# Kernel tuning notes

Measured on AMD Instinct MI355X. Metric: run time of the kernel, lower is better.

## Reference

```python
import jax, jax.numpy as jnp
import numpy as np

EMBED_DIM = 1024
NUM_HEADS = 16
HEAD_DIM = EMBED_DIM // NUM_HEADS
B, S = 4, 2048


def setup_inputs() -> dict:
    key = jax.random.key(0)
    ks = jax.random.split(key, 9)
    s = 1.0 / np.sqrt(EMBED_DIM)
    x = jax.random.normal(ks[0], (B, S, EMBED_DIM), dtype=jnp.float32)
    # nn.Linear weights stored [out, in]; y = x @ W.T + b
    Wq = jax.random.uniform(ks[1], (EMBED_DIM, EMBED_DIM), jnp.float32, -s, s)
    bq = jax.random.uniform(ks[2], (EMBED_DIM,), jnp.float32, -s, s)
    Wk = jax.random.uniform(ks[3], (EMBED_DIM, EMBED_DIM), jnp.float32, -s, s)
    bk = jax.random.uniform(ks[4], (EMBED_DIM,), jnp.float32, -s, s)
    Wv = jax.random.uniform(ks[5], (EMBED_DIM, EMBED_DIM), jnp.float32, -s, s)
    bv = jax.random.uniform(ks[6], (EMBED_DIM,), jnp.float32, -s, s)
    Wo = jax.random.uniform(ks[7], (EMBED_DIM, EMBED_DIM), jnp.float32, -s, s)
    bo = jax.random.uniform(ks[8], (EMBED_DIM,), jnp.float32, -s, s)
    return {"x": x, "Wq": Wq, "bq": bq, "Wk": Wk, "bk": bk,
            "Wv": Wv, "bv": bv, "Wo": Wo, "bo": bo}


def _split_heads(t):
    b, s, _ = t.shape
    return t.reshape(b, s, NUM_HEADS, HEAD_DIM).transpose(0, 2, 1, 3)  # [B,H,S,D]


def reference(x, Wq, bq, Wk, bk, Wv, bv, Wo, bo):
    q = _split_heads(x @ Wq.T + bq)
    k = _split_heads(x @ Wk.T + bk)
    v = _split_heads(x @ Wv.T + bv)
    scores = jnp.einsum('bhqd,bhkd->bhqk', q, k) / np.sqrt(HEAD_DIM)  # [B,H,S,S]
    attn = jax.nn.softmax(scores, axis=-1)
    ctx = jnp.einsum('bhqk,bhkd->bhqd', attn, v)          # [B,H,S,D]
    ctx = ctx.transpose(0, 2, 1, 3).reshape(x.shape[0], x.shape[1], EMBED_DIM)
    return ctx @ Wo.T + bo
```

## Files before the change

kernel.cpp:

```cpp
#include <hip/hip_runtime.h>
#include <hip/hip_bf16.h>
#include <stdint.h>

typedef __attribute__((ext_vector_type(8))) short  bf16x8;
typedef __attribute__((ext_vector_type(4))) float  f32x4;
typedef __attribute__((ext_vector_type(4))) unsigned int u32x4;
typedef __attribute__((ext_vector_type(2))) unsigned int u32x2;

#define LOG2E 1.4426950408889634f

__device__ __forceinline__ unsigned short f2bf(float f) {
  unsigned int u = __builtin_bit_cast(unsigned int, f);
  u += 0x7fffu + ((u >> 16) & 1u);
  return (unsigned short)(u >> 16);
}

__device__ __forceinline__ unsigned int pk2(float a, float b) {
  __hip_bfloat162 h = __float22bfloat162_rn(make_float2(a, b));
  unsigned int u;
  __builtin_memcpy(&u, &h, 4);
  return u;
}

__device__ __forceinline__ void async16(const void* g, void* l) {
  __builtin_amdgcn_global_load_lds(
      (const __attribute__((address_space(1))) unsigned int*)g,
      (__attribute__((address_space(3))) unsigned int*)l,
      16, 0, 0);
}

__global__ __launch_bounds__(256) void cast_all(
    const float* __restrict__ x,
    const float* __restrict__ Wq, const float* __restrict__ Wk,
    const float* __restrict__ Wv, const float* __restrict__ Wo,
    unsigned short* __restrict__ xb, unsigned short* __restrict__ wqkv,
    unsigned short* __restrict__ wo) {
  int i = blockIdx.x * 256 + threadIdx.x;
  const float* src;
  unsigned short* dst;
  int off;
  if (i < 2097152) {
    src = x; dst = xb; off = i;
  } else {
    int j = i - 2097152;
    int seg = j >> 18; off = j & 262143;
    src = (seg == 0) ? Wq : (seg == 1) ? Wk : (seg == 2) ? Wv : Wo;
    dst = (seg < 3) ? (wqkv + (size_t)seg * 1048576) : wo;
  }
  float4 f = ((const float4*)src)[off];
  uint2 o;
  o.x = pk2(f.x, f.y);
  o.y = pk2(f.z, f.w);
  ((uint2*)dst)[off] = o;
}

__global__ __launch_bounds__(256) void gemm_qkv(
    const unsigned short* __restrict__ xb, const unsigned short* __restrict__ wqkv,
    const float* __restrict__ bq, const float* __restrict__ bk, const float* __restrict__ bv,
    unsigned short* __restrict__ qb, unsigned short* __restrict__ kb,
    unsigned short* __restrict__ vb) {
  __shared__ __align__(16) unsigned short As[128 * 32];
  __shared__ __align__(16) unsigned short Bs[128 * 32];
  __shared__ __align__(16) unsigned short epi[4][64 * 72];
  const int bid = blockIdx.x;
  const int xcd = bid & 7, idx = bid >> 3;
  const int nt = xcd * 3 + (idx % 3);
  const int mt = idx / 3;
  const int m0 = mt * 128, n0 = nt * 128;
  const int tid = threadIdx.x;
  const int wv = tid >> 6, lane = tid & 63, qq = lane >> 4, ln = lane & 15;
  const int wm = wv & 1, wn = wv >> 1;
  const int K = 1024;

  f32x4 acc[4][4];
#pragma unroll
  for (int i = 0; i < 4; ++i)
#pragma unroll
    for (int j = 0; j < 4; ++j) acc[i][j] = f32x4{0.f, 0.f, 0.f, 0.f};

  for (int k0 = 0; k0 < K; k0 += 32) {
#pragma unroll
    for (int i = 0; i < 2; ++i) {
      int cc = wv * 2 + i;
      int jp = cc * 64 + lane;
      int row = jp >> 2, cp = jp & 3;
      int c = cp ^ ((row >> 1) & 3);
      async16(xb   + (size_t)(m0 + row) * K + k0 + c * 8, As + cc * 512);
      async16(wqkv + (size_t)(n0 + row) * K + k0 + c * 8, Bs + cc * 512);
    }
    __syncthreads();
    bf16x8 af[4], bf[4];
#pragma unroll
    for (int i = 0; i < 4; ++i) {
      int row = wm * 64 + i * 16 + ln;
      af[i] = *(const bf16x8*)(As + row * 32 + (qq ^ ((row >> 1) & 3)) * 8);
    }
#pragma unroll
    for (int j = 0; j < 4; ++j) {
      int row = wn * 64 + j * 16 + ln;
      bf[j] = *(const bf16x8*)(Bs + row * 32 + (qq ^ ((row >> 1) & 3)) * 8);
    }
#pragma unroll
    for (int i = 0; i < 4; ++i)
#pragma unroll
      for (int j = 0; j < 4; ++j)
        acc[i][j] = __builtin_amdgcn_mfma_f32_16x16x32_bf16(af[i], bf[j], acc[i][j], 0, 0, 0);
    __syncthreads();
  }

  const int nblk = n0 >> 10;
  const float* bias = (nblk == 0) ? bq : (nblk == 1) ? bk : bv;
  const float scale = (nblk == 0) ? (0.125f * LOG2E) : 1.0f;
  unsigned short* buf = epi[wv];
  const int ncol0 = (n0 & 1023) + wn * 64;
  const int head  = ncol0 >> 6;
  const int mbase = m0 + wm * 64;
  const int b     = mbase >> 11, sbase = mbase & 2047;
  unsigned short* dst = (nblk == 0) ? qb : (nblk == 1) ? kb : vb;

  if (nblk != 2) {
#pragma unroll
    for (int j = 0; j < 4; ++j) {
      float bs = bias[ncol0 + j * 16 + ln] * scale;
#pragma unroll
      for (int i = 0; i < 4; ++i)
#pragma unroll
        for (int r = 0; r < 4; ++r)
          buf[(i * 16 + qq * 4 + r) * 72 + j * 16 + ln] = f2bf(acc[i][j][r] * scale + bs);
    }
    unsigned short* gout = dst + (((size_t)(b * 16 + head)) * 2048 + sbase) * 64;
#pragma unroll
    for (int h = 0; h < 2; ++h)
#pragma unroll
      for (int p = 0; p < 4; ++p) {
        int rr = (lane >> 2) + p * 16;
        int c4 = lane & 3;
        ulonglong2 v = *(const ulonglong2*)(buf + rr * 72 + h * 32 + c4 * 8);
        *(ulonglong2*)(gout + (size_t)rr * 64 + h * 32 + c4 * 8) = v;
      }
  } else {
#pragma unroll
    for (int j = 0; j < 4; ++j) {
      float bs = bias[ncol0 + j * 16 + ln];
#pragma unroll
      for (int i = 0; i < 4; ++i) {
        uint2 pk;
        pk.x = pk2(acc[i][j][0] + bs, acc[i][j][1] + bs);
        pk.y = pk2(acc[i][j][2] + bs, acc[i][j][3] + bs);
        *(uint2*)(buf + (j * 16 + ln) * 72 + i * 16 + qq * 4) = pk;
      }
    }
    unsigned short* gout = dst + ((size_t)(b * 16 + head)) * 64 * 2048 + sbase;
#pragma unroll
    for (int p = 0; p < 8; ++p) {
      int dr = (lane >> 3) + p * 8;
      int c8 = lane & 7;
      ulonglong2 v = *(const ulonglong2*)(buf + dr * 72 + c8 * 8);
      *(ulonglong2*)(gout + (size_t)dr * 2048 + c8 * 8) = v;
    }
  }
}

__global__ __launch_bounds__(256, 4) void attn_kernel(
    const unsigned short* __restrict__ qb, const unsigned short* __restrict__ kb,
    const unsigned short* __restrict__ vb, unsigned short* __restrict__ ctx) {
  __shared__ __align__(16) unsigned short k_sh[2][64 * 64];
  __shared__ __align__(16) unsigned short vT_sh[2][64 * 64];
  const int bid = blockIdx.x;
  const int xcd = bid & 7, idx = bid >> 3;
  const int bh = xcd * 8 + (idx >> 4);
  const int q0 = (idx & 15) * 128;
  const int tid = threadIdx.x;
  const int wv = tid >> 6, lane = tid & 63, qq = lane >> 4, ln = lane & 15;

  bf16x8 qf[2][2];
  {
    const unsigned short* qbase = qb + ((size_t)bh * 2048 + q0 + wv * 32) * 64;
#pragma unroll
    for (int rb = 0; rb < 2; ++rb)
#pragma unroll
      for (int kq = 0; kq < 2; ++kq)
        qf[rb][kq] = *(const bf16x8*)(qbase + (rb * 16 + ln) * 64 + kq * 32 + qq * 8);
  }

  f32x4 o_acc[2][4];
  float l_i[2] = {0.f, 0.f};
#pragma unroll
  for (int rb = 0; rb < 2; ++rb)
#pragma unroll
    for (int nt = 0; nt < 4; ++nt) o_acc[rb][nt] = f32x4{0.f, 0.f, 0.f, 0.f};

  const unsigned short* kgbase = kb + (size_t)bh * 2048 * 64;
  const unsigned short* vgbase = vb + (size_t)bh * 64 * 2048;
  const int cc0 = wv * 2;

  auto stageKV = [&](int kt, int buf) {
#pragma unroll
    for (int i = 0; i < 2; ++i) {
      int jp = (cc0 + i) * 64 + lane;
      int row = jp >> 3, c = (jp & 7) ^ (row & 7);
      async16(kgbase + (size_t)(kt * 64 + row) * 64 + c * 8, k_sh[buf] + (cc0 + i) * 512);
      async16(vgbase + (size_t)row * 2048 + kt * 64 + c * 8, vT_sh[buf] + (cc0 + i) * 512);
    }
  };

  stageKV(0, 0);
  asm volatile("s_waitcnt vmcnt(0)" ::: "memory");
  __builtin_amdgcn_s_barrier();

  for (int kt = 0; kt < 32; ++kt) {
    const int cur = kt & 1;
    const unsigned short* kcur = k_sh[cur];
    const unsigned short* vcur = vT_sh[cur];
    if (kt < 31) stageKV(kt + 1, cur ^ 1);

    f32x4 s_acc[2][4];
#pragma unroll
    for (int rb = 0; rb < 2; ++rb)
#pragma unroll
      for (int ct = 0; ct < 4; ++ct) s_acc[rb][ct] = f32x4{0.f, 0.f, 0.f, 0.f};
    __builtin_amdgcn_s_setprio(1);
#pragma unroll
    for (int ct = 0; ct < 4; ++ct) {
      int row = ct * 16 + ln;
      bf16x8 kf0 = *(const bf16x8*)(kcur + row * 64 + ((0 + qq) ^ (row & 7)) * 8);
      bf16x8 kf1 = *(const bf16x8*)(kcur + row * 64 + ((4 + qq) ^ (row & 7)) * 8);
#pragma unroll
      for (int rb = 0; rb < 2; ++rb) {
        s_acc[rb][ct] = __builtin_amdgcn_mfma_f32_16x16x32_bf16(kf0, qf[rb][0], s_acc[rb][ct], 0, 0, 0);
        s_acc[rb][ct] = __builtin_amdgcn_mfma_f32_16x16x32_bf16(kf1, qf[rb][1], s_acc[rb][ct], 0, 0, 0);
      }
    }
    __builtin_amdgcn_s_setprio(0);

    bf16x8 pf[2][2];
#pragma unroll
    for (int rb = 0; rb < 2; ++rb) {
      unsigned int W[4][2];
      float sum = 0.f;
#pragma unroll
      for (int ct = 0; ct < 4; ++ct) {
        float p0 = __builtin_amdgcn_exp2f(s_acc[rb][ct][0]);
        float p1 = __builtin_amdgcn_exp2f(s_acc[rb][ct][1]);
        float p2 = __builtin_amdgcn_exp2f(s_acc[rb][ct][2]);
        float p3 = __builtin_amdgcn_exp2f(s_acc[rb][ct][3]);
        sum += (p0 + p1) + (p2 + p3);
        W[ct][0] = pk2(p0, p1);
        W[ct][1] = pk2(p2, p3);
      }
      l_i[rb] += sum;
#pragma unroll
      for (int kk = 0; kk < 2; ++kk) {
        u32x2 a1 = __builtin_amdgcn_permlane32_swap(W[2 * kk][0], W[2 * kk + 1][0], false, false);
        u32x2 a2 = __builtin_amdgcn_permlane16_swap(a1.x, a1.y, false, false);
        u32x2 b1 = __builtin_amdgcn_permlane32_swap(W[2 * kk][1], W[2 * kk + 1][1], false, false);
        u32x2 b2 = __builtin_amdgcn_permlane16_swap(b1.x, b1.y, false, false);
        u32x4 pw = {a2.x, b2.x, a2.y, b2.y};
        pf[rb][kk] = __builtin_bit_cast(bf16x8, pw);
      }
    }

#pragma unroll
    for (int kk = 0; kk < 2; ++kk) {
      bf16x8 vf[4];
#pragma unroll
      for (int nt = 0; nt < 4; ++nt) {
        int row = nt * 16 + ln;
        vf[nt] = *(const bf16x8*)(vcur + row * 64 + ((kk * 4 + qq) ^ (row & 7)) * 8);
      }
      __builtin_amdgcn_s_setprio(1);
#pragma unroll
      for (int rb = 0; rb < 2; ++rb)
#pragma unroll
        for (int nt = 0; nt < 4; ++nt)
          o_acc[rb][nt] = __builtin_amdgcn_mfma_f32_16x16x32_bf16(vf[nt], pf[rb][kk], o_acc[rb][nt], 0, 0, 0);
      __builtin_amdgcn_s_setprio(0);
    }

    if (kt < 31) asm volatile("s_waitcnt vmcnt(0)" ::: "memory");
    __builtin_amdgcn_s_barrier();
  }

  unsigned short* ep = (unsigned short*)k_sh;
#pragma unroll
  for (int rb = 0; rb < 2; ++rb) {
    l_i[rb] += __shfl_xor(l_i[rb], 16);
    l_i[rb] += __shfl_xor(l_i[rb], 32);
    float inv = 1.0f / l_i[rb];
    int row = wv * 32 + rb * 16 + ln;
    int rs = row & 7;
#pragma unroll
    for (int nt = 0; nt < 4; ++nt) {
      uint2 pk;
      pk.x = pk2(o_acc[rb][nt][0] * inv, o_acc[rb][nt][1] * inv);
      pk.y = pk2(o_acc[rb][nt][2] * inv, o_acc[rb][nt][3] * inv);
      *(uint2*)(ep + row * 64 + (((nt * 2 + (qq >> 1)) ^ rs) << 3) + ((qq & 1) << 2)) = pk;
    }
  }
  {
    const int b = bh >> 4, h = bh & 15;
    int r = tid >> 1, half = tid & 1;
    int rs = r & 7;
    int s = q0 + r;
    size_t gbase = ((size_t)(b * 2048 + s)) * 1024 + h * 64 + half * 32;
    const unsigned short* lsrc = ep + r * 64;
#pragma unroll
    for (int j = 0; j < 4; ++j)
      ((ulonglong2*)(ctx + gbase + j * 8))[0] =
          *(const ulonglong2*)(lsrc + (((half * 4 + j) ^ rs) << 3));
  }
}

__global__ __launch_bounds__(256) void gemm_out(
    const unsigned short* __restrict__ ctx, const unsigned short* __restrict__ wo,
    const float* __restrict__ bo, float* __restrict__ out) {
  __shared__ __align__(16) unsigned short As[2][128 * 32];
  __shared__ __align__(16) unsigned short Bs[2][128 * 32];
  const int bid = blockIdx.x;
  const int n0 = (bid & 7) * 128;
  const int m0 = (bid >> 3) * 128;
  const int tid = threadIdx.x;
  const int wv = tid >> 6, lane = tid & 63, qq = lane >> 4, ln = lane & 15;
  const int wm = wv & 1, wn = wv >> 1;
  const int K = 1024;

  f32x4 acc[4][4];
#pragma unroll
  for (int i = 0; i < 4; ++i)
#pragma unroll
    for (int j = 0; j < 4; ++j) acc[i][j] = f32x4{0.f, 0.f, 0.f, 0.f};

  auto stage = [&](int t, int buf) {
#pragma unroll
    for (int i = 0; i < 2; ++i) {
      int cc = wv * 2 + i;
      int jp = cc * 64 + lane;
      int row = jp >> 2, cp = jp & 3;
      int c = cp ^ ((row >> 1) & 3);
      async16(ctx + (size_t)(m0 + row) * K + t * 32 + c * 8, As[buf] + cc * 512);
      async16(wo  + (size_t)(n0 + row) * K + t * 32 + c * 8, Bs[buf] + cc * 512);
    }
  };

  stage(0, 0);
  for (int t = 0; t < 32; ++t) {
    const int cur = t & 1;
    if (t < 31) {
      stage(t + 1, cur ^ 1);
      asm volatile("s_waitcnt vmcnt(4)" ::: "memory");
    } else {
      asm volatile("s_waitcnt vmcnt(0)" ::: "memory");
    }
    __builtin_amdgcn_s_barrier();

    bf16x8 af[4], bf[4];
#pragma unroll
    for (int i = 0; i < 4; ++i) {
      int row = wm * 64 + i * 16 + ln;
      af[i] = *(const bf16x8*)(As[cur] + row * 32 + (qq ^ ((row >> 1) & 3)) * 8);
    }
#pragma unroll
    for (int j = 0; j < 4; ++j) {
      int row = wn * 64 + j * 16 + ln;
      bf[j] = *(const bf16x8*)(Bs[cur] + row * 32 + (qq ^ ((row >> 1) & 3)) * 8);
    }
#pragma unroll
    for (int i = 0; i < 4; ++i)
#pragma unroll
      for (int j = 0; j < 4; ++j)
        acc[i][j] = __builtin_amdgcn_mfma_f32_16x16x32_bf16(af[i], bf[j], acc[i][j], 0, 0, 0);
    __builtin_amdgcn_s_barrier();
  }

#pragma unroll
  for (int j = 0; j < 4; ++j) {
    int n = n0 + wn * 64 + j * 16 + ln;
    float bsv = bo[n];
#pragma unroll
    for (int i = 0; i < 4; ++i) {
#pragma unroll
      for (int r = 0; r < 4; ++r) {
        int m = m0 + wm * 64 + i * 16 + qq * 4 + r;
        out[(size_t)m * 1024 + n] = acc[i][j][r] + bsv;
      }
    }
  }
}

extern "C" void kernel_launch(void* const* d_in, const int* in_sizes, int n_in,
                              void* d_out, int out_size, void* d_ws, size_t ws_size,
                              hipStream_t stream) {
  const float* x  = (const float*)d_in[0];
  const float* Wq = (const float*)d_in[1];
  const float* bq = (const float*)d_in[2];
  const float* Wk = (const float*)d_in[3];
  const float* bk = (const float*)d_in[4];
  const float* Wv = (const float*)d_in[5];
  const float* bv = (const float*)d_in[6];
  const float* Wo = (const float*)d_in[7];
  const float* bo = (const float*)d_in[8];
  float* out = (float*)d_out;

  char* ws = (char*)d_ws;
  unsigned short* xb   = (unsigned short*)(ws);
  unsigned short* ctxb = (unsigned short*)(ws);
  unsigned short* qb   = (unsigned short*)(ws + ((size_t)16 << 20));
  unsigned short* kbuf = (unsigned short*)(ws + ((size_t)32 << 20));
  unsigned short* vbuf = (unsigned short*)(ws + ((size_t)48 << 20));
  unsigned short* wqkv = (unsigned short*)(ws + ((size_t)64 << 20));
  unsigned short* wo   = (unsigned short*)(ws + ((size_t)70 << 20));

  cast_all<<<12288, 256, 0, stream>>>(x, Wq, Wk, Wv, Wo, xb, wqkv, wo);

  gemm_qkv<<<1536, 256, 0, stream>>>(xb, wqkv, bq, bk, bv, qb, kbuf, vbuf);
  attn_kernel<<<1024, 256, 0, stream>>>(qb, kbuf, vbuf, ctxb);
  gemm_out<<<512, 256, 0, stream>>>(ctxb, wo, bo, out);
}
```

Measured before the change: 297.6 us.

## Double attention query tile per block to reuse K/V tiles across more rows

Each attention block now handles 256 query rows instead of 128, with each wave owning 64 rows (4 row blocks), so K/V tiles staged in shared memory are reused across twice as many queries. The grid halves to 512 blocks and launch bounds drop to 2 blocks per SM to allow the larger register footprint. The S computation is restructured per row block, starting from a zero accumulator with the K fragments loaded once per tile. In exchange it raises register pressure and lowers occupancy and block count, which could hurt latency hiding and load balance across CUs.

```diff
diff --git a/kernel.cpp b/kernel.cpp
--- a/kernel.cpp
+++ b/kernel.cpp
@@ -161,34 +161,34 @@
   }
 }
 
-__global__ __launch_bounds__(256, 4) void attn_kernel(
+__global__ __launch_bounds__(256, 2) void attn_kernel(
     const unsigned short* __restrict__ qb, const unsigned short* __restrict__ kb,
     const unsigned short* __restrict__ vb, unsigned short* __restrict__ ctx) {
-  __shared__ __align__(16) unsigned short k_sh[2][64 * 64];
-  __shared__ __align__(16) unsigned short vT_sh[2][64 * 64];
+  __shared__ __align__(16) unsigned short sh[16384];
   const int bid = blockIdx.x;
   const int xcd = bid & 7, idx = bid >> 3;
-  const int bh = xcd * 8 + (idx >> 4);
-  const int q0 = (idx & 15) * 128;
+  const int bh = xcd * 8 + (idx >> 3);
+  const int q0 = (idx & 7) * 256;
   const int tid = threadIdx.x;
   const int wv = tid >> 6, lane = tid & 63, qq = lane >> 4, ln = lane & 15;
 
-  bf16x8 qf[2][2];
+  bf16x8 qf[4][2];
   {
-    const unsigned short* qbase = qb + ((size_t)bh * 2048 + q0 + wv * 32) * 64;
-#pragma unroll
-    for (int rb = 0; rb < 2; ++rb)
+    const unsigned short* qbase = qb + ((size_t)bh * 2048 + q0 + wv * 64) * 64;
+#pragma unroll
+    for (int rb = 0; rb < 4; ++rb)
 #pragma unroll
       for (int kq = 0; kq < 2; ++kq)
         qf[rb][kq] = *(const bf16x8*)(qbase + (rb * 16 + ln) * 64 + kq * 32 + qq * 8);
   }
 
-  f32x4 o_acc[2][4];
-  float l_i[2] = {0.f, 0.f};
-#pragma unroll
-  for (int rb = 0; rb < 2; ++rb)
+  f32x4 o_acc[4][4];
+  float l_i[4] = {0.f, 0.f, 0.f, 0.f};
+#pragma unroll
+  for (int rb = 0; rb < 4; ++rb)
 #pragma unroll
     for (int nt = 0; nt < 4; ++nt) o_acc[rb][nt] = f32x4{0.f, 0.f, 0.f, 0.f};
+  const f32x4 z4 = f32x4{0.f, 0.f, 0.f, 0.f};
 
   const unsigned short* kgbase = kb + (size_t)bh * 2048 * 64;
   const unsigned short* vgbase = vb + (size_t)bh * 64 * 2048;
@@ -199,8 +199,10 @@
     for (int i = 0; i < 2; ++i) {
       int jp = (cc0 + i) * 64 + lane;
       int row = jp >> 3, c = (jp & 7) ^ (row & 7);
-      async16(kgbase + (size_t)(kt * 64 + row) * 64 + c * 8, k_sh[buf] + (cc0 + i) * 512);
-      async16(vgbase + (size_t)row * 2048 + kt * 64 + c * 8, vT_sh[buf] + (cc0 + i) * 512);
+      async16(kgbase + (size_t)(kt * 64 + row) * 64 + c * 8,
+              sh + buf * 4096 + (cc0 + i) * 512);
+      async16(vgbase + (size_t)row * 2048 + kt * 64 + c * 8,
+              sh + 8192 + buf * 4096 + (cc0 + i) * 512);
     }
   };
 
@@ -210,45 +212,40 @@
 
   for (int kt = 0; kt < 32; ++kt) {
     const int cur = kt & 1;
-    const unsigned short* kcur = k_sh[cur];
-    const unsigned short* vcur = vT_sh[cur];
+    const unsigned short* kcur = sh + cur * 4096;
+    const unsigned short* vcur = sh + 8192 + cur * 4096;
     if (kt < 31) stageKV(kt + 1, cur ^ 1);
 
-    f32x4 s_acc[2][4];
-#pragma unroll
-    for (int rb = 0; rb < 2; ++rb)
-#pragma unroll
-      for (int ct = 0; ct < 4; ++ct) s_acc[rb][ct] = f32x4{0.f, 0.f, 0.f, 0.f};
-    __builtin_amdgcn_s_setprio(1);
+    bf16x8 kf[4][2];
 #pragma unroll
     for (int ct = 0; ct < 4; ++ct) {
       int row = ct * 16 + ln;
-      bf16x8 kf0 = *(const bf16x8*)(kcur + row * 64 + ((0 + qq) ^ (row & 7)) * 8);
-      bf16x8 kf1 = *(const bf16x8*)(kcur + row * 64 + ((4 + qq) ^ (row & 7)) * 8);
-#pragma unroll
-      for (int rb = 0; rb < 2; ++rb) {
-        s_acc[rb][ct] = __builtin_amdgcn_mfma_f32_16x16x32_bf16(kf0, qf[rb][0], s_acc[rb][ct], 0, 0, 0);
-        s_acc[rb][ct] = __builtin_amdgcn_mfma_f32_16x16x32_bf16(kf1, qf[rb][1], s_acc[rb][ct], 0, 0, 0);
-      }
-    }
-    __builtin_amdgcn_s_setprio(0);
-
-    bf16x8 pf[2][2];
-#pragma unroll
-    for (int rb = 0; rb < 2; ++rb) {
+      kf[ct][0] = *(const bf16x8*)(kcur + row * 64 + ((0 + qq) ^ (row & 7)) * 8);
+      kf[ct][1] = *(const bf16x8*)(kcur + row * 64 + ((4 + qq) ^ (row & 7)) * 8);
+    }
+
+    bf16x8 pf[4][2];
+#pragma unroll
+    for (int rb = 0; rb < 4; ++rb) {
+      f32x4 s_acc[4];
+      __builtin_amdgcn_s_setprio(1);
+#pragma unroll
+      for (int ct = 0; ct < 4; ++ct) {
+        s_acc[ct] = __builtin_amdgcn_mfma_f32_16x16x32_bf16(kf[ct][0], qf[rb][0], z4, 0, 0, 0);
+        s_acc[ct] = __builtin_amdgcn_mfma_f32_16x16x32_bf16(kf[ct][1], qf[rb][1], s_acc[ct], 0, 0, 0);
+      }
+      __builtin_amdgcn_s_setprio(0);
       unsigned int W[4][2];
-      float sum = 0.f;
 #pragma unroll
       for (int ct = 0; ct < 4; ++ct) {
-        float p0 = __builtin_amdgcn_exp2f(s_acc[rb][ct][0]);
-        float p1 = __builtin_amdgcn_exp2f(s_acc[rb][ct][1]);
-        float p2 = __builtin_amdgcn_exp2f(s_acc[rb][ct][2]);
-        float p3 = __builtin_amdgcn_exp2f(s_acc[rb][ct][3]);
-        sum += (p0 + p1) + (p2 + p3);
+        float p0 = __builtin_amdgcn_exp2f(s_acc[ct][0]);
+        float p1 = __builtin_amdgcn_exp2f(s_acc[ct][1]);
+        float p2 = __builtin_amdgcn_exp2f(s_acc[ct][2]);
+        float p3 = __builtin_amdgcn_exp2f(s_acc[ct][3]);
+        l_i[rb] += (p0 + p1) + (p2 + p3);
         W[ct][0] = pk2(p0, p1);
         W[ct][1] = pk2(p2, p3);
       }
-      l_i[rb] += sum;
 #pragma unroll
       for (int kk = 0; kk < 2; ++kk) {
         u32x2 a1 = __builtin_amdgcn_permlane32_swap(W[2 * kk][0], W[2 * kk + 1][0], false, false);
@@ -270,7 +267,7 @@
       }
       __builtin_amdgcn_s_setprio(1);
 #pragma unroll
-      for (int rb = 0; rb < 2; ++rb)
+      for (int rb = 0; rb < 4; ++rb)
 #pragma unroll
         for (int nt = 0; nt < 4; ++nt)
           o_acc[rb][nt] = __builtin_amdgcn_mfma_f32_16x16x32_bf16(vf[nt], pf[rb][kk], o_acc[rb][nt], 0, 0, 0);
@@ -281,13 +278,13 @@
     __builtin_amdgcn_s_barrier();
   }
 
-  unsigned short* ep = (unsigned short*)k_sh;
-#pragma unroll
-  for (int rb = 0; rb < 2; ++rb) {
+  unsigned short* ep = sh;
+#pragma unroll
+  for (int rb = 0; rb < 4; ++rb) {
     l_i[rb] += __shfl_xor(l_i[rb], 16);
     l_i[rb] += __shfl_xor(l_i[rb], 32);
     float inv = 1.0f / l_i[rb];
-    int row = wv * 32 + rb * 16 + ln;
+    int row = wv * 64 + rb * 16 + ln;
     int rs = row & 7;
 #pragma unroll
     for (int nt = 0; nt < 4; ++nt) {
@@ -299,15 +296,14 @@
   }
   {
     const int b = bh >> 4, h = bh & 15;
-    int r = tid >> 1, half = tid & 1;
-    int rs = r & 7;
-    int s = q0 + r;
-    size_t gbase = ((size_t)(b * 2048 + s)) * 1024 + h * 64 + half * 32;
+    int r = tid;
+    int rs2 = r & 7;
+    size_t gbase = ((size_t)(b * 2048 + q0 + r)) * 1024 + h * 64;
     const unsigned short* lsrc = ep + r * 64;
 #pragma unroll
-    for (int j = 0; j < 4; ++j)
-      ((ulonglong2*)(ctx + gbase + j * 8))[0] =
-          *(const ulonglong2*)(lsrc + (((half * 4 + j) ^ rs) << 3));
+    for (int j = 0; j < 8; ++j)
+      *(ulonglong2*)(ctx + gbase + (size_t)j * 8) =
+          *(const ulonglong2*)(lsrc + ((j ^ rs2) << 3));
   }
 }
 
@@ -413,6 +409,6 @@
   cast_all<<<12288, 256, 0, stream>>>(x, Wq, Wk, Wv, Wo, xb, wqkv, wo);
 
   gemm_qkv<<<1536, 256, 0, stream>>>(xb, wqkv, bq, bk, bv, qb, kbuf, vbuf);
-  attn_kernel<<<1024, 256, 0, stream>>>(qb, kbuf, vbuf, ctxb);
+  attn_kernel<<<512, 256, 0, stream>>>(qb, kbuf, vbuf, ctxb);
   gemm_out<<<512, 256, 0, stream>>>(ctxb, wo, bo, out);
 }
```

Result: faster. 287.2 us (-3.5%).
